# Kernel tuning notes

Hardware: AMD Instinct MI355X
Metric: run time of the kernel (lower is better)

Reference implementation:

```python
import jax, jax.numpy as jnp
import numpy as np

B, M, N = 128, 512, 512
THRESH = 0.5  # parsed from stop_strategy 'threshold_0.5'
AVG_DEG = 16.0


def setup_inputs() -> dict:
    key = jax.random.key(0)
    k1, k2, k3 = jax.random.split(key, 3)
    y_pred = jax.random.uniform(k1, (B, M, N), dtype=jnp.float32)

    def make_adj(k, n):
        a = (jax.random.uniform(k, (B, n, n)) < (AVG_DEG / n)).astype(jnp.float32)
        a = jnp.maximum(a, jnp.swapaxes(a, 1, 2))          # symmetric
        return a * (1.0 - jnp.eye(n, dtype=jnp.float32))   # no self loops

    return {"y_pred": y_pred, "adj1": make_adj(k2, M), "adj2": make_adj(k3, N)}


def _frontier(adj, v):
    # neighbors of selected nodes that are not yet selected
    return jnp.minimum(adj @ v, 1.0) * (1.0 - v)


def _search_one(y, a1, a2):
    """Greedy MCS tree search for one graph pair. y: (M,N), a1: (M,M), a2: (N,N)."""
    m, n = y.shape

    def cond(s):
        return s[0]

    def body(s):
        cont, v1, v2, tree, fmask = s
        masked = y * fmask
        mx = jnp.max(masked)
        new_cont = mx >= THRESH                 # stop check BEFORE commit (original order)
        idx = jnp.argmax(masked)
        i, j = idx // n, idx % n
        v1n = v1.at[i].set(1.0)
        v2n = v2.at[j].set(1.0)
        treen = tree.at[i, j].set(1.0)
        fmn = _frontier(a1, v1n)[:, None] * _frontier(a2, v2n)[None, :]
        pick = lambda new, old: jnp.where(new_cont, new, old)
        return (new_cont, pick(v1n, v1), pick(v2n, v2), pick(treen, tree), pick(fmn, fmask))

    init = (jnp.array(True),
            jnp.zeros((m,), jnp.float32),
            jnp.zeros((n,), jnp.float32),
            jnp.zeros((m, n), jnp.float32),
            jnp.ones((m, n), jnp.float32))
    final = jax.lax.while_loop(cond, body, init)
    return final[3]  # tree_pred match matrix


@jax.jit
def _search_batch(y_pred, adj1, adj2):
    return jax.vmap(_search_one)(y_pred, adj1, adj2)


def reference(y_pred, adj1, adj2):
    # returns the tree_pred match matrices for every pair in the batch
    return _search_batch(y_pred, adj1, adj2)
```

## Files before the change

kernel.cpp:

```cpp
#include <hip/hip_runtime.h>
#include <stdint.h>

#define MDIM 512
#define NDIM 512
#define NTHREADS 512

typedef unsigned long long u64;

__device__ __forceinline__ u64 wave_max_u64(u64 v) {
#pragma unroll
  for (int off = 32; off; off >>= 1) {
    u64 q = __shfl_xor(v, off);
    if (q > v) v = q;
  }
  return v;
}

__global__ __launch_bounds__(256) void transpose_kernel(
    const float* __restrict__ in, float* __restrict__ out)
{
  __shared__ float tile[32][33];
  const int b = blockIdx.z;
  const float* __restrict__ I = in  + (size_t)b * (MDIM * NDIM);
  float* __restrict__ O       = out + (size_t)b * (MDIM * NDIM);
  const int x  = blockIdx.x * 32 + threadIdx.x;
  const int y0 = blockIdx.y * 32 + threadIdx.y;
#pragma unroll
  for (int dy = 0; dy < 32; dy += 8)
    tile[threadIdx.y + dy][threadIdx.x] = I[(size_t)(y0 + dy) * NDIM + x];
  __syncthreads();
  const int xo = blockIdx.y * 32 + threadIdx.x;
  const int yo = blockIdx.x * 32 + threadIdx.y;
#pragma unroll
  for (int dy = 0; dy < 32; dy += 8)
    O[(size_t)(yo + dy) * MDIM + xo] = tile[threadIdx.x][threadIdx.y + dy];
}

__global__ __launch_bounds__(NTHREADS, 1) void tree_search_kernel(
    const float* __restrict__ y,
    const float* __restrict__ yt,
    const float* __restrict__ a1,
    const float* __restrict__ a2,
    float* __restrict__ out)
{
  const int b   = blockIdx.x;
  const int tid = threadIdx.x;
  const float* __restrict__ Y  = y  + (size_t)b * (MDIM * NDIM);
  const float* __restrict__ YT = yt ? yt + (size_t)b * (MDIM * NDIM) : nullptr;
  const float* __restrict__ A1 = a1 + (size_t)b * (MDIM * MDIM);
  const float* __restrict__ A2 = a2 + (size_t)b * (NDIM * NDIM);
  float* __restrict__ O = out + (size_t)b * (MDIM * NDIM);

  __shared__ unsigned rowState[MDIM];
  __shared__ float    rowMax[MDIM];
  __shared__ unsigned rowArg[MDIM];
  __shared__ unsigned colState[NDIM];
  __shared__ unsigned colList[NDIM];
  __shared__ unsigned colPos[NDIM];
  __shared__ unsigned newCols[NDIM];
  __shared__ unsigned addRows[MDIM];
  __shared__ int s_colCount, s_nAdd, s_nNew, s_stop, s_ci, s_cj;
  __shared__ u64 s_part[NTHREADS / 64];

  rowState[tid] = 0u;
  colState[tid] = 0u;
  rowMax[tid]   = 0.f;
  rowArg[tid]   = 511u;
  if (tid == 0) { s_colCount = 0; s_nAdd = 0; s_nNew = 0; s_stop = 0; }
  __syncthreads();

  {
    u64 best = 0;
    for (int base = tid * 4; base < MDIM * NDIM; base += NTHREADS * 4) {
      const float4 v = *reinterpret_cast<const float4*>(Y + base);
      const float vv[4] = {v.x, v.y, v.z, v.w};
#pragma unroll
      for (int c = 0; c < 4; ++c) {
        u64 p = ((u64)__float_as_uint(vv[c]) << 32)
                | (u64)(262143u - (unsigned)(base + c));
        if (p > best) best = p;
      }
    }
    best = wave_max_u64(best);
    if ((tid & 63) == 0) s_part[tid >> 6] = best;
    __syncthreads();
    if (tid == 0) {
      u64 bst = s_part[0];
#pragma unroll
      for (int w = 1; w < NTHREADS / 64; ++w) if (s_part[w] > bst) bst = s_part[w];
      float v = __uint_as_float((unsigned)(bst >> 32));
      if (v >= 0.5f) {
        unsigned key = 262143u - (unsigned)(bst & 0xFFFFFFFFu);
        int bi = key >> 9, bj = key & 511;
        rowState[bi] = 3u;
        colState[bj] = 2u;
        O[key] = 1.0f;
        s_ci = bi; s_cj = bj;
      } else {
        s_stop = 1;
      }
    }
    __syncthreads();
  }

  while (!s_stop) {
    {
      const int r = tid;
      const unsigned st = rowState[r];
      const float av = A1[(size_t)s_ci * MDIM + r];
      const bool newRow   = (av != 0.f) && (st == 0u);
      const bool recompute = (st == 1u) && (rowArg[r] == (unsigned)s_cj);
      if (newRow || recompute) {
        rowState[r] = 2u;
        addRows[atomicAdd(&s_nAdd, 1)] = (unsigned)r;
      }
      const float bv = A2[(size_t)s_cj * NDIM + r];
      if (bv != 0.f && colState[r] == 0u) {
        colState[r] = 1u;
        newCols[atomicAdd(&s_nNew, 1)] = (unsigned)r;
        int p = atomicAdd(&s_colCount, 1);
        colList[p] = (unsigned)r;
        colPos[r]  = (unsigned)p;
      }
    }
    __syncthreads();

    {
      const int r = tid;
      const bool active = (rowState[r] == 1u);
      float rm = rowMax[r];
      unsigned ra = rowArg[r];
      const int nn = s_nNew;
      if (YT) {
        for (int k = 0; k < nn; ++k) {
          const unsigned c = newCols[k];
          const float v = YT[((unsigned)c << 9) + (unsigned)r];
          if (active && (v > rm || (v == rm && c < ra))) { rm = v; ra = c; }
        }
      } else {
        for (int k = 0; k < nn; ++k) {
          const unsigned c = newCols[k];
          const float v = Y[((unsigned)r << 9) + c];
          if (active && (v > rm || (v == rm && c < ra))) { rm = v; ra = c; }
        }
      }
      if (active) { rowMax[r] = rm; rowArg[r] = ra; }
    }
    __syncthreads();

    {
      const int g = tid >> 3, lane = tid & 7;
      const int nAdd = s_nAdd, cc = s_colCount;
      for (int a = g; a < nAdd; a += NTHREADS / 8) {
        const int rr = (int)addRows[a];
        float rm = 0.f;
        unsigned ra = 511u;
        for (int k = lane; k < cc; k += 8) {
          const unsigned c = colList[k];
          const float v = Y[((unsigned)rr << 9) + c];
          if (v > rm || (v == rm && c < ra)) { rm = v; ra = c; }
        }
        u64 p = ((u64)__float_as_uint(rm) << 32) | (u64)(511u - ra);
#pragma unroll
        for (int off = 4; off; off >>= 1) {
          u64 q = __shfl_xor(p, off, 8);
          if (q > p) p = q;
        }
        if (lane == 0) {
          rowMax[rr]   = __uint_as_float((unsigned)(p >> 32));
          rowArg[rr]   = 511u - (unsigned)(p & 0xFFFFFFFFu);
          rowState[rr] = 1u;
        }
      }
    }
    __syncthreads();

    {
      u64 cand = 0;
      if (rowState[tid] == 1u) {
        const unsigned key = ((unsigned)tid << 9) | rowArg[tid];
        cand = ((u64)__float_as_uint(rowMax[tid]) << 32)
               | (u64)(262143u - key);
      }
      cand = wave_max_u64(cand);
      if ((tid & 63) == 0) s_part[tid >> 6] = cand;
    }
    __syncthreads();

    if (tid == 0) {
      u64 bst = s_part[0];
#pragma unroll
      for (int w = 1; w < NTHREADS / 64; ++w) if (s_part[w] > bst) bst = s_part[w];
      const float v = __uint_as_float((unsigned)(bst >> 32));
      if (v >= 0.5f) {
        const unsigned key = 262143u - (unsigned)(bst & 0xFFFFFFFFu);
        const int bi = key >> 9, bj = key & 511;
        rowState[bi] = 3u;
        colState[bj] = 2u;
        const int p    = (int)colPos[bj];
        const int last = (int)colList[s_colCount - 1];
        colList[p]    = (unsigned)last;
        colPos[last]  = (unsigned)p;
        s_colCount--;
        O[key] = 1.0f;
        s_ci = bi; s_cj = bj;
        s_nAdd = 0; s_nNew = 0;
      } else {
        s_stop = 1;
      }
    }
    __syncthreads();
  }
}

extern "C" void kernel_launch(void* const* d_in, const int* in_sizes, int n_in,
                              void* d_out, int out_size, void* d_ws, size_t ws_size,
                              hipStream_t stream) {
  const float* y  = (const float*)d_in[0];
  const float* a1 = (const float*)d_in[1];
  const float* a2 = (const float*)d_in[2];
  float* out = (float*)d_out;
  const int B = in_sizes[0] / (MDIM * NDIM);

  (void)hipMemsetAsync(d_out, 0, (size_t)out_size * sizeof(float), stream);

  const size_t yt_bytes = (size_t)B * MDIM * NDIM * sizeof(float);
  float* yt = nullptr;
  if (ws_size >= yt_bytes) {
    yt = (float*)d_ws;
    dim3 tb(32, 8, 1), tg(NDIM / 32, MDIM / 32, B);
    transpose_kernel<<<tg, tb, 0, stream>>>(y, yt);
  }
  tree_search_kernel<<<B, NTHREADS, 0, stream>>>(y, yt, a1, a2, out);
}
```

Measured before the change: 3.701 ms.

## Cache adjacency as LDS bitmasks and merge per-iteration phases to cut barriers

Each adjacency matrix is packed into shared-memory bitmasks with wave ballots at kernel start, so the per-step neighbour lookups no longer read global memory. The incremental update of new columns and the full recompute of added rows now run in one phase. The argmax uses a persistent packed-key array reduced by a single wave, dropping two barriers per greedy step. This adds an upfront pass over both adjacency matrices and uses roughly 80KB more LDS per block.

```diff
diff --git a/kernel.cpp b/kernel.cpp
--- a/kernel.cpp
+++ b/kernel.cpp
@@ -51,6 +51,9 @@
   const float* __restrict__ A2 = a2 + (size_t)b * (NDIM * NDIM);
   float* __restrict__ O = out + (size_t)b * (MDIM * NDIM);
 
+  __shared__ u64 a1bits[MDIM * 8];
+  __shared__ u64 a2bits[NDIM * 8];
+  __shared__ u64 s_packed[MDIM];
   __shared__ unsigned rowState[MDIM];
   __shared__ float    rowMax[MDIM];
   __shared__ unsigned rowArg[MDIM];
@@ -62,10 +65,36 @@
   __shared__ int s_colCount, s_nAdd, s_nNew, s_stop, s_ci, s_cj;
   __shared__ u64 s_part[NTHREADS / 64];
 
-  rowState[tid] = 0u;
-  colState[tid] = 0u;
-  rowMax[tid]   = 0.f;
-  rowArg[tid]   = 511u;
+  const int wave = tid >> 6, lane = tid & 63;
+
+  for (int r = wave; r < MDIM; r += NTHREADS / 64) {
+    const float* row = A1 + (size_t)r * MDIM;
+    float vals[8];
+#pragma unroll
+    for (int w = 0; w < 8; ++w) vals[w] = row[(w << 6) + lane];
+#pragma unroll
+    for (int w = 0; w < 8; ++w) {
+      u64 m = __ballot(vals[w] != 0.f);
+      if (lane == 0) a1bits[(r << 3) + w] = m;
+    }
+  }
+  for (int r = wave; r < NDIM; r += NTHREADS / 64) {
+    const float* row = A2 + (size_t)r * NDIM;
+    float vals[8];
+#pragma unroll
+    for (int w = 0; w < 8; ++w) vals[w] = row[(w << 6) + lane];
+#pragma unroll
+    for (int w = 0; w < 8; ++w) {
+      u64 m = __ballot(vals[w] != 0.f);
+      if (lane == 0) a2bits[(r << 3) + w] = m;
+    }
+  }
+
+  rowState[tid]  = 0u;
+  colState[tid]  = 0u;
+  rowMax[tid]    = 0.f;
+  rowArg[tid]    = 511u;
+  s_packed[tid]  = 0ull;
   if (tid == 0) { s_colCount = 0; s_nAdd = 0; s_nNew = 0; s_stop = 0; }
   __syncthreads();
 
@@ -82,7 +111,7 @@
       }
     }
     best = wave_max_u64(best);
-    if ((tid & 63) == 0) s_part[tid >> 6] = best;
+    if (lane == 0) s_part[wave] = best;
     __syncthreads();
     if (tid == 0) {
       u64 bst = s_part[0];
@@ -104,18 +133,20 @@
   }
 
   while (!s_stop) {
+    bool iActive;
     {
       const int r = tid;
       const unsigned st = rowState[r];
-      const float av = A1[(size_t)s_ci * MDIM + r];
-      const bool newRow   = (av != 0.f) && (st == 0u);
-      const bool recompute = (st == 1u) && (rowArg[r] == (unsigned)s_cj);
-      if (newRow || recompute) {
+      const int radj = (int)((a1bits[((unsigned)s_ci << 3) + (r >> 6)] >> (r & 63)) & 1ull);
+      const bool newRow = radj && (st == 0u);
+      const bool recomp = (st == 1u) && (rowArg[r] == (unsigned)s_cj);
+      iActive = (st == 1u) && !recomp;
+      if (newRow || recomp) {
         rowState[r] = 2u;
         addRows[atomicAdd(&s_nAdd, 1)] = (unsigned)r;
       }
-      const float bv = A2[(size_t)s_cj * NDIM + r];
-      if (bv != 0.f && colState[r] == 0u) {
+      const int cadj = (int)((a2bits[((unsigned)s_cj << 3) + (r >> 6)] >> (r & 63)) & 1ull);
+      if (cadj && colState[r] == 0u) {
         colState[r] = 1u;
         newCols[atomicAdd(&s_nNew, 1)] = (unsigned)r;
         int p = atomicAdd(&s_colCount, 1);
@@ -126,36 +157,29 @@
     __syncthreads();
 
     {
-      const int r = tid;
-      const bool active = (rowState[r] == 1u);
-      float rm = rowMax[r];
-      unsigned ra = rowArg[r];
-      const int nn = s_nNew;
-      if (YT) {
-        for (int k = 0; k < nn; ++k) {
-          const unsigned c = newCols[k];
-          const float v = YT[((unsigned)c << 9) + (unsigned)r];
-          if (active && (v > rm || (v == rm && c < ra))) { rm = v; ra = c; }
-        }
-      } else {
-        for (int k = 0; k < nn; ++k) {
-          const unsigned c = newCols[k];
-          const float v = Y[((unsigned)r << 9) + c];
-          if (active && (v > rm || (v == rm && c < ra))) { rm = v; ra = c; }
-        }
-      }
-      if (active) { rowMax[r] = rm; rowArg[r] = ra; }
-    }
-    __syncthreads();
-
-    {
-      const int g = tid >> 3, lane = tid & 7;
-      const int nAdd = s_nAdd, cc = s_colCount;
-      for (int a = g; a < nAdd; a += NTHREADS / 8) {
+      if (iActive) {
+        const int nn = s_nNew;
+        if (nn > 0) {
+          float rm = rowMax[tid];
+          unsigned ra = rowArg[tid];
+          for (int k = 0; k < nn; ++k) {
+            const unsigned c = newCols[k];
+            const float v = YT ? YT[(c << 9) + (unsigned)tid]
+                               : Y[((unsigned)tid << 9) + c];
+            if (v > rm || (v == rm && c < ra)) { rm = v; ra = c; }
+          }
+          rowMax[tid] = rm; rowArg[tid] = ra;
+          s_packed[tid] = ((u64)__float_as_uint(rm) << 32)
+                        | (u64)(262143u - (((unsigned)tid << 9) | ra));
+        }
+      }
+      const int g = tid >> 3, lane8 = tid & 7;
+      const int nA = s_nAdd, cc = s_colCount;
+      for (int a = g; a < nA; a += NTHREADS / 8) {
         const int rr = (int)addRows[a];
         float rm = 0.f;
         unsigned ra = 511u;
-        for (int k = lane; k < cc; k += 8) {
+        for (int k = lane8; k < cc; k += 8) {
           const unsigned c = colList[k];
           const float v = Y[((unsigned)rr << 9) + c];
           if (v > rm || (v == rm && c < ra)) { rm = v; ra = c; }
@@ -166,47 +190,46 @@
           u64 q = __shfl_xor(p, off, 8);
           if (q > p) p = q;
         }
-        if (lane == 0) {
-          rowMax[rr]   = __uint_as_float((unsigned)(p >> 32));
-          rowArg[rr]   = 511u - (unsigned)(p & 0xFFFFFFFFu);
+        if (lane8 == 0) {
+          const unsigned vb = (unsigned)(p >> 32);
+          const unsigned rb = 511u - (unsigned)(p & 0xFFFFFFFFu);
+          rowMax[rr]   = __uint_as_float(vb);
+          rowArg[rr]   = rb;
           rowState[rr] = 1u;
-        }
-      }
-    }
-    __syncthreads();
-
-    {
-      u64 cand = 0;
-      if (rowState[tid] == 1u) {
-        const unsigned key = ((unsigned)tid << 9) | rowArg[tid];
-        cand = ((u64)__float_as_uint(rowMax[tid]) << 32)
-               | (u64)(262143u - key);
-      }
-      cand = wave_max_u64(cand);
-      if ((tid & 63) == 0) s_part[tid >> 6] = cand;
-    }
-    __syncthreads();
-
-    if (tid == 0) {
-      u64 bst = s_part[0];
-#pragma unroll
-      for (int w = 1; w < NTHREADS / 64; ++w) if (s_part[w] > bst) bst = s_part[w];
-      const float v = __uint_as_float((unsigned)(bst >> 32));
-      if (v >= 0.5f) {
-        const unsigned key = 262143u - (unsigned)(bst & 0xFFFFFFFFu);
-        const int bi = key >> 9, bj = key & 511;
-        rowState[bi] = 3u;
-        colState[bj] = 2u;
-        const int p    = (int)colPos[bj];
-        const int last = (int)colList[s_colCount - 1];
-        colList[p]    = (unsigned)last;
-        colPos[last]  = (unsigned)p;
-        s_colCount--;
-        O[key] = 1.0f;
-        s_ci = bi; s_cj = bj;
-        s_nAdd = 0; s_nNew = 0;
-      } else {
-        s_stop = 1;
+          s_packed[rr] = ((u64)vb << 32)
+                       | (u64)(262143u - (((unsigned)rr << 9) | rb));
+        }
+      }
+    }
+    __syncthreads();
+
+    if (tid < 64) {
+      u64 best = 0;
+#pragma unroll
+      for (int k = 0; k < MDIM / 64; ++k) {
+        const u64 q = s_packed[tid + (k << 6)];
+        if (q > best) best = q;
+      }
+      best = wave_max_u64(best);
+      if (tid == 0) {
+        const float v = __uint_as_float((unsigned)(best >> 32));
+        if (v >= 0.5f) {
+          const unsigned key = 262143u - (unsigned)(best & 0xFFFFFFFFu);
+          const int bi = key >> 9, bj = key & 511;
+          rowState[bi] = 3u;
+          s_packed[bi] = 0ull;
+          colState[bj] = 2u;
+          const int p    = (int)colPos[bj];
+          const int last = (int)colList[s_colCount - 1];
+          colList[p]    = (unsigned)last;
+          colPos[last]  = (unsigned)p;
+          s_colCount--;
+          O[key] = 1.0f;
+          s_ci = bi; s_cj = bj;
+          s_nAdd = 0; s_nNew = 0;
+        } else {
+          s_stop = 1;
+        }
       }
     }
     __syncthreads();
```

Measured after the change: 3.291 ms. 11.1% less time.
